# Optimization experiments

Hardware: AMD Instinct MI355X
Metric: run time of the kernel (lower is better)

The kernel has to match this reference:

```python
import math
import jax, jax.numpy as jnp
import numpy as np

B, L, D_M, H, D_K, D_V = 2, 2048, 1024, 16, 64, 64


def setup_inputs() -> dict:
    key = jax.random.key(0)
    ks = jax.random.split(key, 12)
    s_in = 1.0 / math.sqrt(D_M)
    s_cat = 1.0 / math.sqrt(H * D_V)
    return {
        "Q": jax.random.normal(ks[0], (B, L, D_M), jnp.float32),
        "K": jax.random.normal(ks[1], (B, L, D_M), jnp.float32),
        "V": jax.random.normal(ks[2], (B, L, D_M), jnp.float32),
        # per-head projections batched along a leading head axis
        "Wq": jax.random.uniform(ks[3], (H, D_M, D_K), jnp.float32, -s_in, s_in),
        "bq": jax.random.uniform(ks[4], (H, D_K), jnp.float32, -s_in, s_in),
        "Wk": jax.random.uniform(ks[5], (H, D_M, D_K), jnp.float32, -s_in, s_in),
        "bk": jax.random.uniform(ks[6], (H, D_K), jnp.float32, -s_in, s_in),
        "Wv": jax.random.uniform(ks[7], (H, D_M, D_V), jnp.float32, -s_in, s_in),
        "bv": jax.random.uniform(ks[8], (H, D_V), jnp.float32, -s_in, s_in),
        "Wo": jax.random.uniform(ks[9], (H * D_V, D_M), jnp.float32, -s_cat, s_cat),
        "bo": jax.random.uniform(ks[10], (D_M,), jnp.float32, -s_cat, s_cat),
    }


def reference(Q, K, V, Wq, bq, Wk, bk, Wv, bv, Wo, bo):
    # Batched per-head projections: [B,L,Dm] x [H,Dm,Dk] -> [B,H,L,Dk]
    Qp = jnp.einsum("bqm,hmk->bhqk", Q, Wq) + bq[None, :, None, :]
    Kp = jnp.einsum("bsm,hmk->bhsk", K, Wk) + bk[None, :, None, :]
    Vp = jnp.einsum("bsm,hmv->bhsv", V, Wv) + bv[None, :, None, :]
    scores = jnp.einsum("bhqk,bhsk->bhqs", Qp, Kp) / jnp.sqrt(
        jnp.asarray(D_K, Qp.dtype)
    )
    # NOTE: original torch code uses Softmax(dim=1) on a [B,Lq,Lk] matrix,
    # i.e. normalization over the QUERY axis (axis=2 here), not the key axis.
    attn = jax.nn.softmax(scores, axis=2)
    wV = jnp.einsum("bhqs,bhsv->bhqv", attn, Vp)  # [B,H,Lq,Dv]
    cat_V = jnp.transpose(wV, (0, 2, 1, 3)).reshape(B, L, H * D_V)
    return cat_V @ Wo + bo
```

## Files before the change

### kernel.cpp

```cpp
#include <hip/hip_runtime.h>
#include <hip/hip_bf16.h>

#define DEVI __device__ __forceinline__

typedef __hip_bfloat16 bf16;
typedef __attribute__((ext_vector_type(8))) __bf16 bf16x8;
typedef __attribute__((ext_vector_type(4))) float f32x4;
typedef __attribute__((ext_vector_type(4))) short short4v;
typedef __attribute__((ext_vector_type(8))) short short8v;


DEVI short bfbits(float f) { bf16 h = __float2bfloat16(f); return *(short*)&h; }

DEVI void gl16(const void* g, void* l) {
  __builtin_amdgcn_global_load_lds((const __attribute__((address_space(1))) void*)g,
                                   (__attribute__((address_space(3))) void*)l, 16, 0, 0);
}

DEVI f32x4 MF(bf16x8 a, bf16x8 b, f32x4 c) {
  return __builtin_amdgcn_mfma_f32_16x16x32_bf16(a, b, c, 0, 0, 0);
}

__global__ __launch_bounds__(256) void k_cvt_qkv(
    const float* __restrict__ Q, const float* __restrict__ K, const float* __restrict__ V,
    bf16* __restrict__ Qb, bf16* __restrict__ Kb, bf16* __restrict__ Vb) {
  const float* s = blockIdx.y == 0 ? Q : (blockIdx.y == 1 ? K : V);
  bf16* d = blockIdx.y == 0 ? Qb : (blockIdx.y == 1 ? Kb : Vb);
  int i = (blockIdx.x * 256 + threadIdx.x) * 4;
  float4 v = *(const float4*)(s + i);
  short4v o;
  o[0] = bfbits(v.x); o[1] = bfbits(v.y); o[2] = bfbits(v.z); o[3] = bfbits(v.w);
  *(short4v*)(d + i) = o;
}

__global__ __launch_bounds__(256) void k_prep_w(
    const float* __restrict__ Wq, const float* __restrict__ Wk, const float* __restrict__ Wv,
    const float* __restrict__ Wo,
    bf16* __restrict__ WqT, bf16* __restrict__ WkT, bf16* __restrict__ WvT,
    bf16* __restrict__ WoT) {
  __shared__ float t[64][65];
  const int z = blockIdx.z;
  const float* in; bf16* out; int ldin, ldout;
  if (z < 3) {
    const float* W = z == 0 ? Wq : (z == 1 ? Wk : Wv);
    bf16* O = z == 0 ? WqT : (z == 1 ? WkT : WvT);
    const int hh = blockIdx.y, m0 = blockIdx.x * 64;
    in = W + hh * 65536 + m0 * 64; ldin = 64;
    out = O + hh * 65536 + m0;     ldout = 1024;
  } else {
    const int r0 = blockIdx.x * 64, c0 = blockIdx.y * 64;
    in = Wo + r0 * 1024 + c0; ldin = 1024;
    out = WoT + c0 * 1024 + r0; ldout = 1024;
  }
  const int tx = threadIdx.x & 63, ty = threadIdx.x >> 6;
  for (int r = ty; r < 64; r += 4) t[r][tx] = in[r * ldin + tx];
  __syncthreads();
  for (int c = ty; c < 64; c += 4) out[c * ldout + tx] = __float2bfloat16(t[tx][c]);
}

__global__ __launch_bounds__(256) void k_proj_gemm(
    const bf16* __restrict__ Qb, const bf16* __restrict__ Kb, const bf16* __restrict__ Vb,
    const bf16* __restrict__ WqT, const bf16* __restrict__ WkT, const bf16* __restrict__ WvT,
    const float* __restrict__ bq, const float* __restrict__ bk, const float* __restrict__ bv,
    bf16* __restrict__ Qp, bf16* __restrict__ Kp, bf16* __restrict__ VpT) {
  __shared__ bf16 As[128 * 64], Bs[128 * 64];
  const int z = blockIdx.z;
  const bf16* A  = z == 0 ? Qb : (z == 1 ? Kb : Vb);
  const bf16* BT = z == 0 ? WqT : (z == 1 ? WkT : WvT);
  const float* bias = z == 0 ? bq : (z == 1 ? bk : bv);
  const int row0 = blockIdx.x * 128, col0 = blockIdx.y * 128;
  const int tid = threadIdx.x, lane = tid & 63, wave = tid >> 6;
  const int wq = wave >> 1, wn = wave & 1;
  f32x4 acc[4][4];
#pragma unroll
  for (int i = 0; i < 4; ++i)
#pragma unroll
    for (int j = 0; j < 4; ++j) acc[i][j] = (f32x4)0.0f;

  for (int k0 = 0; k0 < 1024; k0 += 64) {
#pragma unroll
    for (int it = 0; it < 4; ++it) {
      int boff = (it * 4 + wave) * 1024 + lane * 16;
      int r = boff >> 7, cb = boff & 127;
      gl16((const char*)A  + (size_t)(row0 + r) * 2048 + k0 * 2 + cb, (char*)As + boff);
      gl16((const char*)BT + (size_t)(col0 + r) * 2048 + k0 * 2 + cb, (char*)Bs + boff);
    }
    __syncthreads();
#pragma unroll
    for (int ks = 0; ks < 2; ++ks) {
      bf16x8 a[4], b[4];
#pragma unroll
      for (int i = 0; i < 4; ++i)
        a[i] = *(const bf16x8*)&As[(wq * 64 + i * 16 + (lane & 15)) * 64 + ks * 32 + (lane >> 4) * 8];
#pragma unroll
      for (int j = 0; j < 4; ++j)
        b[j] = *(const bf16x8*)&Bs[(wn * 64 + j * 16 + (lane & 15)) * 64 + ks * 32 + (lane >> 4) * 8];
#pragma unroll
      for (int i = 0; i < 4; ++i)
#pragma unroll
        for (int j = 0; j < 4; ++j) acc[i][j] = MF(a[i], b[j], acc[i][j]);
    }
    __syncthreads();
  }

  if (z < 2) {
    bf16* C = z == 0 ? Qp : Kp;
#pragma unroll
    for (int i = 0; i < 4; ++i)
#pragma unroll
      for (int j = 0; j < 4; ++j) {
        int col = col0 + wn * 64 + j * 16 + (lane & 15);
        float bb = bias[col];
#pragma unroll
        for (int r = 0; r < 4; ++r) {
          int row = row0 + wq * 64 + i * 16 + (lane >> 4) * 4 + r;
          C[row * 1024 + col] = __float2bfloat16(acc[i][j][r] + bb);
        }
      }
  } else {
    const int b = row0 >> 11, lr = row0 & 2047;
#pragma unroll
    for (int i = 0; i < 4; ++i)
#pragma unroll
      for (int j = 0; j < 4; ++j) {
        int n = col0 + wn * 64 + j * 16 + (lane & 15);
        float bb = bias[n];
        int s0 = lr + wq * 64 + i * 16 + (lane >> 4) * 4;
        short4v o;
#pragma unroll
        for (int r = 0; r < 4; ++r) o[r] = bfbits(acc[i][j][r] + bb);
        *(short4v*)&VpT[((b * 16 + (n >> 6)) * 64 + (n & 63)) * 2048 + s0] = o;
      }
  }
}

__global__ __launch_bounds__(256) void k_stats(
    const bf16* __restrict__ Qp, const bf16* __restrict__ Kp, float* __restrict__ lc) {
  __shared__ bf16 Ks[128 * 64], Qs[64 * 64];
  const int s0 = blockIdx.x * 128, bh = blockIdx.y;
  const int b = bh >> 4, h = bh & 15;
  const char* Qrow = (const char*)(Qp + (b * 2048) * 1024 + h * 64);
  const char* Krow = (const char*)(Kp + (b * 2048) * 1024 + h * 64);
  const int tid = threadIdx.x, lane = tid & 63, wave = tid >> 6;
#pragma unroll
  for (int it = 0; it < 4; ++it) {
    int boff = (it * 4 + wave) * 1024 + lane * 16;
    int r = boff >> 7, cb = boff & 127;
    gl16(Krow + (size_t)(s0 + r) * 2048 + cb, (char*)Ks + boff);
  }
  __syncthreads();
  bf16x8 afr[2][2];
#pragma unroll
  for (int sf = 0; sf < 2; ++sf)
#pragma unroll
    for (int ks = 0; ks < 2; ++ks)
      afr[sf][ks] = *(const bf16x8*)&Ks[(wave * 32 + sf * 16 + (lane & 15)) * 64 + ks * 32 + (lane >> 4) * 8];
  float zr[2][4] = {{0.f, 0.f, 0.f, 0.f}, {0.f, 0.f, 0.f, 0.f}};

  for (int q0 = 0; q0 < 2048; q0 += 64) {
    __syncthreads();
#pragma unroll
    for (int it = 0; it < 2; ++it) {
      int boff = (it * 4 + wave) * 1024 + lane * 16;
      int r = boff >> 7, cb = boff & 127;
      gl16(Qrow + (size_t)(q0 + r) * 2048 + cb, (char*)Qs + boff);
    }
    __syncthreads();
    f32x4 acc[2][4];
#pragma unroll
    for (int sf = 0; sf < 2; ++sf)
#pragma unroll
      for (int qf = 0; qf < 4; ++qf) acc[sf][qf] = (f32x4)0.0f;
#pragma unroll
    for (int ks = 0; ks < 2; ++ks) {
      bf16x8 bfr[4];
#pragma unroll
      for (int qf = 0; qf < 4; ++qf)
        bfr[qf] = *(const bf16x8*)&Qs[(qf * 16 + (lane & 15)) * 64 + ks * 32 + (lane >> 4) * 8];
#pragma unroll
      for (int sf = 0; sf < 2; ++sf)
#pragma unroll
        for (int qf = 0; qf < 4; ++qf) acc[sf][qf] = MF(afr[sf][ks], bfr[qf], acc[sf][qf]);
    }
#pragma unroll
    for (int sf = 0; sf < 2; ++sf)
#pragma unroll
      for (int qf = 0; qf < 4; ++qf)
#pragma unroll
        for (int r = 0; r < 4; ++r) zr[sf][r] += __expf(acc[sf][qf][r] * 0.125f);
  }
#pragma unroll
  for (int m = 1; m <= 8; m <<= 1)
#pragma unroll
    for (int sf = 0; sf < 2; ++sf)
#pragma unroll
      for (int r = 0; r < 4; ++r) zr[sf][r] += __shfl_xor(zr[sf][r], m);
  if ((lane & 15) == 0) {
#pragma unroll
    for (int sf = 0; sf < 2; ++sf)
#pragma unroll
      for (int r = 0; r < 4; ++r)
        lc[bh * 2048 + s0 + wave * 32 + sf * 16 + (lane >> 4) * 4 + r] = -__logf(zr[sf][r]);
  }
}

__global__ __launch_bounds__(256) void k_attn_pv(
    const bf16* __restrict__ Qp, const bf16* __restrict__ Kp, const bf16* __restrict__ VpT,
    const float* __restrict__ lc, bf16* __restrict__ wV) {
  __shared__ bf16 Qs[128 * 64];
  __shared__ bf16 Ks[64 * 64];
  __shared__ bf16 Vs[64 * 64];
  __shared__ bf16 Ps[128 * 72];
  __shared__ float lcs[64];
  const int q0 = blockIdx.x * 128, bh = blockIdx.y;
  const int b = bh >> 4, h = bh & 15;
  const char* Qrow = (const char*)(Qp + (b * 2048) * 1024 + h * 64);
  const char* Krow = (const char*)(Kp + (b * 2048) * 1024 + h * 64);
  const char* Vrow = (const char*)(VpT + bh * 64 * 2048);
  const float* lcb = lc + bh * 2048;
  const int tid = threadIdx.x, lane = tid & 63, wave = tid >> 6;

#pragma unroll
  for (int it = 0; it < 4; ++it) {
    int boff = (it * 4 + wave) * 1024 + lane * 16;
    int r = boff >> 7, cb = boff & 127;
    gl16(Qrow + (size_t)(q0 + r) * 2048 + cb, (char*)Qs + boff);
  }
  __syncthreads();
  bf16x8 aq[2][2];
#pragma unroll
  for (int qf = 0; qf < 2; ++qf)
#pragma unroll
    for (int ks = 0; ks < 2; ++ks)
      aq[qf][ks] = *(const bf16x8*)&Qs[(wave * 32 + qf * 16 + (lane & 15)) * 64 + ks * 32 + (lane >> 4) * 8];

  f32x4 acco[2][4];
#pragma unroll
  for (int qf = 0; qf < 2; ++qf)
#pragma unroll
    for (int vf = 0; vf < 4; ++vf) acco[qf][vf] = (f32x4)0.0f;

  for (int sc = 0; sc < 2048; sc += 64) {
    __syncthreads();
#pragma unroll
    for (int it = 0; it < 2; ++it) {
      int boff = (it * 4 + wave) * 1024 + lane * 16;
      int r = boff >> 7, cb = boff & 127;
      gl16(Krow + (size_t)(sc + r) * 2048 + cb, (char*)Ks + boff);
      gl16(Vrow + (size_t)r * 4096 + sc * 2 + cb, (char*)Vs + boff);
    }
    if (tid < 64) lcs[tid] = lcb[sc + tid];
    __syncthreads();

    f32x4 sacc[2][4];
#pragma unroll
    for (int qf = 0; qf < 2; ++qf)
#pragma unroll
      for (int sf = 0; sf < 4; ++sf) sacc[qf][sf] = (f32x4)0.0f;
#pragma unroll
    for (int ks = 0; ks < 2; ++ks) {
      bf16x8 bk_[4];
#pragma unroll
      for (int sf = 0; sf < 4; ++sf)
        bk_[sf] = *(const bf16x8*)&Ks[(sf * 16 + (lane & 15)) * 64 + ks * 32 + (lane >> 4) * 8];
#pragma unroll
      for (int qf = 0; qf < 2; ++qf)
#pragma unroll
        for (int sf = 0; sf < 4; ++sf) sacc[qf][sf] = MF(aq[qf][ks], bk_[sf], sacc[qf][sf]);
    }
#pragma unroll
    for (int qf = 0; qf < 2; ++qf)
#pragma unroll
      for (int sf = 0; sf < 4; ++sf) {
        int sl = sf * 16 + (lane & 15);
        float lcv = lcs[sl];
#pragma unroll
        for (int r = 0; r < 4; ++r) {
          float p = __expf(sacc[qf][sf][r] * 0.125f + lcv);
          Ps[(wave * 32 + qf * 16 + (lane >> 4) * 4 + r) * 72 + sl] = __float2bfloat16(p);
        }
      }
#pragma unroll
    for (int ks = 0; ks < 2; ++ks) {
      bf16x8 pa[2], pb[4];
#pragma unroll
      for (int qf = 0; qf < 2; ++qf)
        pa[qf] = *(const bf16x8*)&Ps[(wave * 32 + qf * 16 + (lane & 15)) * 72 + ks * 32 + (lane >> 4) * 8];
#pragma unroll
      for (int vf = 0; vf < 4; ++vf)
        pb[vf] = *(const bf16x8*)&Vs[(vf * 16 + (lane & 15)) * 64 + ks * 32 + (lane >> 4) * 8];
#pragma unroll
      for (int qf = 0; qf < 2; ++qf)
#pragma unroll
        for (int vf = 0; vf < 4; ++vf) acco[qf][vf] = MF(pa[qf], pb[vf], acco[qf][vf]);
    }
  }
#pragma unroll
  for (int qf = 0; qf < 2; ++qf)
#pragma unroll
    for (int vf = 0; vf < 4; ++vf) {
      int v = vf * 16 + (lane & 15);
#pragma unroll
      for (int r = 0; r < 4; ++r)
        Ps[(wave * 32 + qf * 16 + (lane >> 4) * 4 + r) * 72 + v] = __float2bfloat16(acco[qf][vf][r]);
    }
  __syncthreads();
  {
    int r = tid >> 1, p = tid & 1;
    char* dst = (char*)(wV + (bh * 2048 + q0 + r) * 64 + p * 32);
#pragma unroll
    for (int i = 0; i < 4; ++i) {
      short8v x = *(const short8v*)&Ps[r * 72 + p * 32 + i * 8];
      *(short8v*)(dst + i * 16) = x;
    }
  }
}

__global__ __launch_bounds__(256) void k_out_gemm(
    const bf16* __restrict__ wV, const bf16* __restrict__ WoT, const float* __restrict__ bo,
    float* __restrict__ out) {
  __shared__ bf16 As[128 * 64], Bs[128 * 64];
  const int row0 = blockIdx.x * 128, col0 = blockIdx.y * 128;
  const int tid = threadIdx.x, lane = tid & 63, wave = tid >> 6;
  const int wq = wave >> 1, wn = wave & 1;
  const int b = row0 >> 11, lr = row0 & 2047;
  f32x4 acc[4][4];
#pragma unroll
  for (int i = 0; i < 4; ++i)
#pragma unroll
    for (int j = 0; j < 4; ++j) acc[i][j] = (f32x4)0.0f;

  for (int k0 = 0; k0 < 1024; k0 += 64) {
    const char* Abase = (const char*)(wV + ((b * 16 + (k0 >> 6)) * 2048 + lr) * 64);
#pragma unroll
    for (int it = 0; it < 4; ++it) {
      int boff = (it * 4 + wave) * 1024 + lane * 16;
      int r = boff >> 7, cb = boff & 127;
      gl16(Abase + boff, (char*)As + boff);
      gl16((const char*)WoT + (size_t)(col0 + r) * 2048 + k0 * 2 + cb, (char*)Bs + boff);
    }
    __syncthreads();
#pragma unroll
    for (int ks = 0; ks < 2; ++ks) {
      bf16x8 a[4], bb[4];
#pragma unroll
      for (int i = 0; i < 4; ++i)
        a[i] = *(const bf16x8*)&As[(wq * 64 + i * 16 + (lane & 15)) * 64 + ks * 32 + (lane >> 4) * 8];
#pragma unroll
      for (int j = 0; j < 4; ++j)
        bb[j] = *(const bf16x8*)&Bs[(wn * 64 + j * 16 + (lane & 15)) * 64 + ks * 32 + (lane >> 4) * 8];
#pragma unroll
      for (int i = 0; i < 4; ++i)
#pragma unroll
        for (int j = 0; j < 4; ++j) acc[i][j] = MF(a[i], bb[j], acc[i][j]);
    }
    __syncthreads();
  }
#pragma unroll
  for (int i = 0; i < 4; ++i)
#pragma unroll
    for (int j = 0; j < 4; ++j) {
      int col = col0 + wn * 64 + j * 16 + (lane & 15);
      float bb = bo[col];
#pragma unroll
      for (int r = 0; r < 4; ++r) {
        int row = row0 + wq * 64 + i * 16 + (lane >> 4) * 4 + r;
        out[row * 1024 + col] = acc[i][j][r] + bb;
      }
    }
}

extern "C" void kernel_launch(void* const* d_in, const int* in_sizes, int n_in,
                              void* d_out, int out_size, void* d_ws, size_t ws_size,
                              hipStream_t stream) {
  (void)in_sizes; (void)n_in; (void)out_size; (void)ws_size;
  const float* Q  = (const float*)d_in[0];
  const float* K  = (const float*)d_in[1];
  const float* V  = (const float*)d_in[2];
  const float* Wq = (const float*)d_in[3];
  const float* bq = (const float*)d_in[4];
  const float* Wk = (const float*)d_in[5];
  const float* bk = (const float*)d_in[6];
  const float* Wv = (const float*)d_in[7];
  const float* bv = (const float*)d_in[8];
  const float* Wo = (const float*)d_in[9];
  const float* bo = (const float*)d_in[10];

  char* ws = (char*)d_ws;
  bf16* Qb  = (bf16*)(ws);
  bf16* Kb  = (bf16*)(ws + (8u  << 20));
  bf16* Vb  = (bf16*)(ws + (16u << 20));
  bf16* WqT = (bf16*)(ws + (24u << 20));
  bf16* WkT = (bf16*)(ws + (26u << 20));
  bf16* WvT = (bf16*)(ws + (28u << 20));
  bf16* WoT = (bf16*)(ws + (30u << 20));
  bf16* Qp  = (bf16*)(ws + (32u << 20));
  bf16* Kp  = (bf16*)(ws + (40u << 20));
  bf16* VpT = (bf16*)(ws + (48u << 20));
  bf16* wVn = (bf16*)(ws + (56u << 20));
  float* lc = (float*)(ws + (64u << 20));

  k_cvt_qkv <<<dim3(4096, 3), 256, 0, stream>>>(Q, K, V, Qb, Kb, Vb);
  k_prep_w  <<<dim3(16, 16, 4), 256, 0, stream>>>(Wq, Wk, Wv, Wo, WqT, WkT, WvT, WoT);
  k_proj_gemm<<<dim3(32, 8, 3), 256, 0, stream>>>(Qb, Kb, Vb, WqT, WkT, WvT, bq, bk, bv, Qp, Kp, VpT);
  k_stats   <<<dim3(16, 32), 256, 0, stream>>>(Qp, Kp, lc);
  k_attn_pv <<<dim3(16, 32), 256, 0, stream>>>(Qp, Kp, VpT, lc, wVn);
  k_out_gemm<<<dim3(32, 8), 256, 0, stream>>>(wVn, WoT, bo, (float*)d_out);
}
```

Baseline: 306.3 us.

## Swizzle LDS tiles, fold softmax normalizer into V, double-buffer attention kernels

Applies an XOR swizzle to all LDS tiles to avoid bank conflicts. Folds the 1/8 scale into Qp and moves the per-key normalizer into a rescale of VpT, so the attention kernel only computes exp(s). It also stages the VpT transpose through LDS for coalesced stores, double-buffers the K/V/Q tiles, and moves the attention kernels to 512-thread blocks with a swizzled block order. The risks are skipping max-subtraction in exp, which could overflow on other inputs, and an extra bf16 rounding of V.

Result: faster. 262.5 us (-14.3%).

```diff
diff --git a/kernel.cpp b/kernel.cpp
--- a/kernel.cpp
+++ b/kernel.cpp
@@ -11,6 +11,7 @@
 
 
 DEVI short bfbits(float f) { bf16 h = __float2bfloat16(f); return *(short*)&h; }
+DEVI float b2f(short s) { union { float f; unsigned u; } c; c.u = ((unsigned)(unsigned short)s) << 16; return c.f; }
 
 DEVI void gl16(const void* g, void* l) {
   __builtin_amdgcn_global_load_lds((const __attribute__((address_space(1))) void*)g,
@@ -20,6 +21,9 @@
 DEVI f32x4 MF(bf16x8 a, bf16x8 b, f32x4 c) {
   return __builtin_amdgcn_mfma_f32_16x16x32_bf16(a, b, c, 0, 0, 0);
 }
+
+DEVI int swzE(int row, int ec) { return row * 64 + (ec ^ ((row & 7) << 3)); }
+DEVI int srcC(int boff) { return (boff & 127) ^ (((boff >> 7) & 7) << 4); }
 
 __global__ __launch_bounds__(256) void k_cvt_qkv(
     const float* __restrict__ Q, const float* __restrict__ K, const float* __restrict__ V,
@@ -63,7 +67,9 @@
     const bf16* __restrict__ WqT, const bf16* __restrict__ WkT, const bf16* __restrict__ WvT,
     const float* __restrict__ bq, const float* __restrict__ bk, const float* __restrict__ bv,
     bf16* __restrict__ Qp, bf16* __restrict__ Kp, bf16* __restrict__ VpT) {
-  __shared__ bf16 As[128 * 64], Bs[128 * 64];
+  __shared__ bf16 smem[17408];
+  bf16* As = smem;
+  bf16* Bs = smem + 8192;
   const int z = blockIdx.z;
   const bf16* A  = z == 0 ? Qb : (z == 1 ? Kb : Vb);
   const bf16* BT = z == 0 ? WqT : (z == 1 ? WkT : WvT);
@@ -81,9 +87,9 @@
 #pragma unroll
     for (int it = 0; it < 4; ++it) {
       int boff = (it * 4 + wave) * 1024 + lane * 16;
-      int r = boff >> 7, cb = boff & 127;
-      gl16((const char*)A  + (size_t)(row0 + r) * 2048 + k0 * 2 + cb, (char*)As + boff);
-      gl16((const char*)BT + (size_t)(col0 + r) * 2048 + k0 * 2 + cb, (char*)Bs + boff);
+      int r = boff >> 7, c = srcC(boff);
+      gl16((const char*)A  + (size_t)(row0 + r) * 2048 + k0 * 2 + c, (char*)As + boff);
+      gl16((const char*)BT + (size_t)(col0 + r) * 2048 + k0 * 2 + c, (char*)Bs + boff);
     }
     __syncthreads();
 #pragma unroll
@@ -91,10 +97,10 @@
       bf16x8 a[4], b[4];
 #pragma unroll
       for (int i = 0; i < 4; ++i)
-        a[i] = *(const bf16x8*)&As[(wq * 64 + i * 16 + (lane & 15)) * 64 + ks * 32 + (lane >> 4) * 8];
+        a[i] = *(const bf16x8*)&As[swzE(wq * 64 + i * 16 + (lane & 15), ks * 32 + (lane >> 4) * 8)];
 #pragma unroll
       for (int j = 0; j < 4; ++j)
-        b[j] = *(const bf16x8*)&Bs[(wn * 64 + j * 16 + (lane & 15)) * 64 + ks * 32 + (lane >> 4) * 8];
+        b[j] = *(const bf16x8*)&Bs[swzE(wn * 64 + j * 16 + (lane & 15), ks * 32 + (lane >> 4) * 8)];
 #pragma unroll
       for (int i = 0; i < 4; ++i)
 #pragma unroll
@@ -104,6 +110,7 @@
   }
 
   if (z < 2) {
+    const float scl = (z == 0) ? 0.125f : 1.0f;
     bf16* C = z == 0 ? Qp : Kp;
 #pragma unroll
     for (int i = 0; i < 4; ++i)
@@ -114,205 +121,203 @@
 #pragma unroll
         for (int r = 0; r < 4; ++r) {
           int row = row0 + wq * 64 + i * 16 + (lane >> 4) * 4 + r;
-          C[row * 1024 + col] = __float2bfloat16(acc[i][j][r] + bb);
+          C[row * 1024 + col] = __float2bfloat16((acc[i][j][r] + bb) * scl);
         }
       }
   } else {
+    bf16* T = smem;
+#pragma unroll
+    for (int i = 0; i < 4; ++i)
+#pragma unroll
+      for (int j = 0; j < 4; ++j) {
+        int nl = wn * 64 + j * 16 + (lane & 15);
+        float bb = bias[col0 + nl];
+#pragma unroll
+        for (int r = 0; r < 4; ++r) {
+          int sl = wq * 64 + i * 16 + (lane >> 4) * 4 + r;
+          T[nl * 136 + sl] = __float2bfloat16(acc[i][j][r] + bb);
+        }
+      }
+    __syncthreads();
     const int b = row0 >> 11, lr = row0 & 2047;
-#pragma unroll
-    for (int i = 0; i < 4; ++i)
-#pragma unroll
-      for (int j = 0; j < 4; ++j) {
-        int n = col0 + wn * 64 + j * 16 + (lane & 15);
-        float bb = bias[n];
-        int s0 = lr + wq * 64 + i * 16 + (lane >> 4) * 4;
-        short4v o;
-#pragma unroll
-        for (int r = 0; r < 4; ++r) o[r] = bfbits(acc[i][j][r] + bb);
-        *(short4v*)&VpT[((b * 16 + (n >> 6)) * 64 + (n & 63)) * 2048 + s0] = o;
-      }
-  }
-}
-
-__global__ __launch_bounds__(256) void k_stats(
-    const bf16* __restrict__ Qp, const bf16* __restrict__ Kp, float* __restrict__ lc) {
-  __shared__ bf16 Ks[128 * 64], Qs[64 * 64];
-  const int s0 = blockIdx.x * 128, bh = blockIdx.y;
+    const int nl = tid >> 1, half = tid & 1;
+    const int n = col0 + nl;
+    bf16* drow = VpT + ((size_t)(b * 16 + (n >> 6)) * 64 + (n & 63)) * 2048 + lr + half * 64;
+#pragma unroll
+    for (int k = 0; k < 8; ++k)
+      *(short8v*)(drow + k * 8) = *(const short8v*)&T[nl * 136 + half * 64 + k * 8];
+  }
+}
+
+__global__ __launch_bounds__(512, 4) void k_stats(
+    const bf16* __restrict__ Qp, const bf16* __restrict__ Kp, bf16* __restrict__ VpT) {
+  __shared__ bf16 Ks[128 * 64];
+  __shared__ bf16 Qs[2][64 * 64];
+  __shared__ float zs[128];
+  const int id = blockIdx.x;
+  const int sw = (id & 7) * 64 + (id >> 3);
+  const int bh = sw >> 4, s0 = (sw & 15) * 128;
   const int b = bh >> 4, h = bh & 15;
-  const char* Qrow = (const char*)(Qp + (b * 2048) * 1024 + h * 64);
-  const char* Krow = (const char*)(Kp + (b * 2048) * 1024 + h * 64);
+  const char* Qrow = (const char*)(Qp + (size_t)(b * 2048) * 1024 + h * 64);
+  const char* Krow = (const char*)(Kp + (size_t)(b * 2048) * 1024 + h * 64);
   const int tid = threadIdx.x, lane = tid & 63, wave = tid >> 6;
-#pragma unroll
-  for (int it = 0; it < 4; ++it) {
-    int boff = (it * 4 + wave) * 1024 + lane * 16;
-    int r = boff >> 7, cb = boff & 127;
-    gl16(Krow + (size_t)(s0 + r) * 2048 + cb, (char*)Ks + boff);
+
+  {
+    int boff = tid * 16;
+#pragma unroll
+    for (int it = 0; it < 2; ++it) {
+      int bo = boff + it * 8192;
+      gl16(Krow + (size_t)(s0 + (bo >> 7)) * 2048 + srcC(bo), (char*)Ks + bo);
+    }
+    gl16(Qrow + (size_t)(boff >> 7) * 2048 + srcC(boff), (char*)Qs[0] + boff);
   }
   __syncthreads();
-  bf16x8 afr[2][2];
-#pragma unroll
-  for (int sf = 0; sf < 2; ++sf)
-#pragma unroll
-    for (int ks = 0; ks < 2; ++ks)
-      afr[sf][ks] = *(const bf16x8*)&Ks[(wave * 32 + sf * 16 + (lane & 15)) * 64 + ks * 32 + (lane >> 4) * 8];
-  float zr[2][4] = {{0.f, 0.f, 0.f, 0.f}, {0.f, 0.f, 0.f, 0.f}};
-
-  for (int q0 = 0; q0 < 2048; q0 += 64) {
-    __syncthreads();
-#pragma unroll
-    for (int it = 0; it < 2; ++it) {
-      int boff = (it * 4 + wave) * 1024 + lane * 16;
-      int r = boff >> 7, cb = boff & 127;
-      gl16(Qrow + (size_t)(q0 + r) * 2048 + cb, (char*)Qs + boff);
-    }
-    __syncthreads();
-    f32x4 acc[2][4];
-#pragma unroll
-    for (int sf = 0; sf < 2; ++sf)
-#pragma unroll
-      for (int qf = 0; qf < 4; ++qf) acc[sf][qf] = (f32x4)0.0f;
+  bf16x8 afr[2];
+#pragma unroll
+  for (int ks = 0; ks < 2; ++ks)
+    afr[ks] = *(const bf16x8*)&Ks[swzE(wave * 16 + (lane & 15), ks * 32 + (lane >> 4) * 8)];
+
+  float zr[4] = {0.f, 0.f, 0.f, 0.f};
+  for (int c = 0; c < 32; ++c) {
+    const int p = c & 1;
+    if (c < 31) {
+      int boff = tid * 16;
+      gl16(Qrow + (size_t)((c + 1) * 64 + (boff >> 7)) * 2048 + srcC(boff), (char*)Qs[p ^ 1] + boff);
+    }
+    f32x4 acc[4];
+#pragma unroll
+    for (int qf = 0; qf < 4; ++qf) acc[qf] = (f32x4)0.0f;
 #pragma unroll
     for (int ks = 0; ks < 2; ++ks) {
       bf16x8 bfr[4];
 #pragma unroll
       for (int qf = 0; qf < 4; ++qf)
-        bfr[qf] = *(const bf16x8*)&Qs[(qf * 16 + (lane & 15)) * 64 + ks * 32 + (lane >> 4) * 8];
-#pragma unroll
-      for (int sf = 0; sf < 2; ++sf)
-#pragma unroll
-        for (int qf = 0; qf < 4; ++qf) acc[sf][qf] = MF(afr[sf][ks], bfr[qf], acc[sf][qf]);
-    }
-#pragma unroll
-    for (int sf = 0; sf < 2; ++sf)
-#pragma unroll
-      for (int qf = 0; qf < 4; ++qf)
-#pragma unroll
-        for (int r = 0; r < 4; ++r) zr[sf][r] += __expf(acc[sf][qf][r] * 0.125f);
+        bfr[qf] = *(const bf16x8*)&Qs[p][swzE(qf * 16 + (lane & 15), ks * 32 + (lane >> 4) * 8)];
+#pragma unroll
+      for (int qf = 0; qf < 4; ++qf) acc[qf] = MF(afr[ks], bfr[qf], acc[qf]);
+    }
+#pragma unroll
+    for (int qf = 0; qf < 4; ++qf)
+#pragma unroll
+      for (int r = 0; r < 4; ++r) zr[r] += __expf(acc[qf][r]);
+    __syncthreads();
   }
 #pragma unroll
   for (int m = 1; m <= 8; m <<= 1)
 #pragma unroll
-    for (int sf = 0; sf < 2; ++sf)
-#pragma unroll
-      for (int r = 0; r < 4; ++r) zr[sf][r] += __shfl_xor(zr[sf][r], m);
+    for (int r = 0; r < 4; ++r) zr[r] += __shfl_xor(zr[r], m);
   if ((lane & 15) == 0) {
 #pragma unroll
-    for (int sf = 0; sf < 2; ++sf)
-#pragma unroll
-      for (int r = 0; r < 4; ++r)
-        lc[bh * 2048 + s0 + wave * 32 + sf * 16 + (lane >> 4) * 4 + r] = -__logf(zr[sf][r]);
-  }
-}
-
-__global__ __launch_bounds__(256) void k_attn_pv(
+    for (int r = 0; r < 4; ++r) zs[wave * 16 + (lane >> 4) * 4 + r] = 1.0f / zr[r];
+  }
+  __syncthreads();
+  {
+    const int v = tid >> 3, seg = tid & 7;
+    bf16* base = VpT + (size_t)(bh * 64 + v) * 2048 + s0 + seg * 16;
+    short8v x0 = *(const short8v*)base;
+    short8v x1 = *(const short8v*)(base + 8);
+    short8v o0, o1;
+#pragma unroll
+    for (int j = 0; j < 8; ++j) {
+      o0[j] = bfbits(b2f(x0[j]) * zs[seg * 16 + j]);
+      o1[j] = bfbits(b2f(x1[j]) * zs[seg * 16 + 8 + j]);
+    }
+    *(short8v*)base = o0;
+    *(short8v*)(base + 8) = o1;
+  }
+}
+
+__global__ __launch_bounds__(512, 4) void k_attn_pv(
     const bf16* __restrict__ Qp, const bf16* __restrict__ Kp, const bf16* __restrict__ VpT,
-    const float* __restrict__ lc, bf16* __restrict__ wV) {
-  __shared__ bf16 Qs[128 * 64];
-  __shared__ bf16 Ks[64 * 64];
-  __shared__ bf16 Vs[64 * 64];
-  __shared__ bf16 Ps[128 * 72];
-  __shared__ float lcs[64];
-  const int q0 = blockIdx.x * 128, bh = blockIdx.y;
+    bf16* __restrict__ wV) {
+  __shared__ bf16 QPs[128 * 64];
+  __shared__ bf16 Ks[2][64 * 64];
+  __shared__ bf16 Vs[2][64 * 64];
+  const int id = blockIdx.x;
+  const int sw = (id & 7) * 64 + (id >> 3);
+  const int bh = sw >> 4, q0 = (sw & 15) * 128;
   const int b = bh >> 4, h = bh & 15;
-  const char* Qrow = (const char*)(Qp + (b * 2048) * 1024 + h * 64);
-  const char* Krow = (const char*)(Kp + (b * 2048) * 1024 + h * 64);
-  const char* Vrow = (const char*)(VpT + bh * 64 * 2048);
-  const float* lcb = lc + bh * 2048;
+  const char* Qrow = (const char*)(Qp + (size_t)(b * 2048) * 1024 + h * 64);
+  const char* Krow = (const char*)(Kp + (size_t)(b * 2048) * 1024 + h * 64);
+  const char* Vrow = (const char*)(VpT + (size_t)bh * 64 * 2048);
   const int tid = threadIdx.x, lane = tid & 63, wave = tid >> 6;
 
-#pragma unroll
-  for (int it = 0; it < 4; ++it) {
-    int boff = (it * 4 + wave) * 1024 + lane * 16;
-    int r = boff >> 7, cb = boff & 127;
-    gl16(Qrow + (size_t)(q0 + r) * 2048 + cb, (char*)Qs + boff);
+  {
+    int boff = tid * 16;
+#pragma unroll
+    for (int it = 0; it < 2; ++it) {
+      int bo = boff + it * 8192;
+      gl16(Qrow + (size_t)(q0 + (bo >> 7)) * 2048 + srcC(bo), (char*)QPs + bo);
+    }
+    gl16(Krow + (size_t)(boff >> 7) * 2048 + srcC(boff), (char*)Ks[0] + boff);
+    gl16(Vrow + (size_t)(boff >> 7) * 4096 + srcC(boff), (char*)Vs[0] + boff);
   }
   __syncthreads();
-  bf16x8 aq[2][2];
-#pragma unroll
-  for (int qf = 0; qf < 2; ++qf)
-#pragma unroll
-    for (int ks = 0; ks < 2; ++ks)
-      aq[qf][ks] = *(const bf16x8*)&Qs[(wave * 32 + qf * 16 + (lane & 15)) * 64 + ks * 32 + (lane >> 4) * 8];
-
-  f32x4 acco[2][4];
-#pragma unroll
-  for (int qf = 0; qf < 2; ++qf)
-#pragma unroll
-    for (int vf = 0; vf < 4; ++vf) acco[qf][vf] = (f32x4)0.0f;
-
-  for (int sc = 0; sc < 2048; sc += 64) {
-    __syncthreads();
-#pragma unroll
-    for (int it = 0; it < 2; ++it) {
-      int boff = (it * 4 + wave) * 1024 + lane * 16;
-      int r = boff >> 7, cb = boff & 127;
-      gl16(Krow + (size_t)(sc + r) * 2048 + cb, (char*)Ks + boff);
-      gl16(Vrow + (size_t)r * 4096 + sc * 2 + cb, (char*)Vs + boff);
-    }
-    if (tid < 64) lcs[tid] = lcb[sc + tid];
-    __syncthreads();
-
-    f32x4 sacc[2][4];
-#pragma unroll
-    for (int qf = 0; qf < 2; ++qf)
-#pragma unroll
-      for (int sf = 0; sf < 4; ++sf) sacc[qf][sf] = (f32x4)0.0f;
+  bf16x8 aq[2];
+#pragma unroll
+  for (int ks = 0; ks < 2; ++ks)
+    aq[ks] = *(const bf16x8*)&QPs[swzE(wave * 16 + (lane & 15), ks * 32 + (lane >> 4) * 8)];
+
+  f32x4 acco[4];
+#pragma unroll
+  for (int vf = 0; vf < 4; ++vf) acco[vf] = (f32x4)0.0f;
+
+  for (int c = 0; c < 32; ++c) {
+    const int p = c & 1;
+    if (c < 31) {
+      int boff = tid * 16;
+      gl16(Krow + (size_t)((c + 1) * 64 + (boff >> 7)) * 2048 + srcC(boff), (char*)Ks[p ^ 1] + boff);
+      gl16(Vrow + (size_t)(boff >> 7) * 4096 + (c + 1) * 128 + srcC(boff), (char*)Vs[p ^ 1] + boff);
+    }
+    f32x4 sacc[4];
+#pragma unroll
+    for (int sf = 0; sf < 4; ++sf) sacc[sf] = (f32x4)0.0f;
 #pragma unroll
     for (int ks = 0; ks < 2; ++ks) {
       bf16x8 bk_[4];
 #pragma unroll
       for (int sf = 0; sf < 4; ++sf)
-        bk_[sf] = *(const bf16x8*)&Ks[(sf * 16 + (lane & 15)) * 64 + ks * 32 + (lane >> 4) * 8];
-#pragma unroll
-      for (int qf = 0; qf < 2; ++qf)
-#pragma unroll
-        for (int sf = 0; sf < 4; ++sf) sacc[qf][sf] = MF(aq[qf][ks], bk_[sf], sacc[qf][sf]);
-    }
-#pragma unroll
-    for (int qf = 0; qf < 2; ++qf)
-#pragma unroll
-      for (int sf = 0; sf < 4; ++sf) {
-        int sl = sf * 16 + (lane & 15);
-        float lcv = lcs[sl];
-#pragma unroll
-        for (int r = 0; r < 4; ++r) {
-          float p = __expf(sacc[qf][sf][r] * 0.125f + lcv);
-          Ps[(wave * 32 + qf * 16 + (lane >> 4) * 4 + r) * 72 + sl] = __float2bfloat16(p);
-        }
+        bk_[sf] = *(const bf16x8*)&Ks[p][swzE(sf * 16 + (lane & 15), ks * 32 + (lane >> 4) * 8)];
+#pragma unroll
+      for (int sf = 0; sf < 4; ++sf) sacc[sf] = MF(aq[ks], bk_[sf], sacc[sf]);
+    }
+#pragma unroll
+    for (int sf = 0; sf < 4; ++sf) {
+      int sl = sf * 16 + (lane & 15);
+#pragma unroll
+      for (int r = 0; r < 4; ++r) {
+        int row = wave * 16 + (lane >> 4) * 4 + r;
+        QPs[swzE(row, sl)] = __float2bfloat16(__expf(sacc[sf][r]));
       }
+    }
 #pragma unroll
     for (int ks = 0; ks < 2; ++ks) {
-      bf16x8 pa[2], pb[4];
-#pragma unroll
-      for (int qf = 0; qf < 2; ++qf)
-        pa[qf] = *(const bf16x8*)&Ps[(wave * 32 + qf * 16 + (lane & 15)) * 72 + ks * 32 + (lane >> 4) * 8];
+      bf16x8 pa = *(const bf16x8*)&QPs[swzE(wave * 16 + (lane & 15), ks * 32 + (lane >> 4) * 8)];
+      bf16x8 pb[4];
 #pragma unroll
       for (int vf = 0; vf < 4; ++vf)
-        pb[vf] = *(const bf16x8*)&Vs[(vf * 16 + (lane & 15)) * 64 + ks * 32 + (lane >> 4) * 8];
-#pragma unroll
-      for (int qf = 0; qf < 2; ++qf)
-#pragma unroll
-        for (int vf = 0; vf < 4; ++vf) acco[qf][vf] = MF(pa[qf], pb[vf], acco[qf][vf]);
-    }
-  }
-#pragma unroll
-  for (int qf = 0; qf < 2; ++qf)
-#pragma unroll
-    for (int vf = 0; vf < 4; ++vf) {
-      int v = vf * 16 + (lane & 15);
-#pragma unroll
-      for (int r = 0; r < 4; ++r)
-        Ps[(wave * 32 + qf * 16 + (lane >> 4) * 4 + r) * 72 + v] = __float2bfloat16(acco[qf][vf][r]);
-    }
-  __syncthreads();
+        pb[vf] = *(const bf16x8*)&Vs[p][swzE(vf * 16 + (lane & 15), ks * 32 + (lane >> 4) * 8)];
+#pragma unroll
+      for (int vf = 0; vf < 4; ++vf) acco[vf] = MF(pa, pb[vf], acco[vf]);
+    }
+    __syncthreads();
+  }
+
+#pragma unroll
+  for (int vf = 0; vf < 4; ++vf) {
+    int v = vf * 16 + (lane & 15);
+#pragma unroll
+    for (int r = 0; r < 4; ++r)
+      QPs[swzE(wave * 16 + (lane >> 4) * 4 + r, v)] = __float2bfloat16(acco[vf][r]);
+  }
   {
-    int r = tid >> 1, p = tid & 1;
-    char* dst = (char*)(wV + (bh * 2048 + q0 + r) * 64 + p * 32);
-#pragma unroll
-    for (int i = 0; i < 4; ++i) {
-      short8v x = *(const short8v*)&Ps[r * 72 + p * 32 + i * 8];
-      *(short8v*)(dst + i * 16) = x;
-    }
+    const int rr = wave * 16 + (lane >> 2);
+    const int x = (rr & 7) << 3;
+    short8v x0 = *(const short8v*)&QPs[rr * 64 + (((lane & 3) * 16) ^ x)];
+    short8v x1 = *(const short8v*)&QPs[rr * 64 + (((lane & 3) * 16 + 8) ^ x)];
+    bf16* dst = wV + ((size_t)bh * 2048 + q0 + rr) * 64 + (lane & 3) * 16;
+    *(short8v*)dst = x0;
+    *(short8v*)(dst + 8) = x1;
   }
 }
 
@@ -331,13 +336,13 @@
     for (int j = 0; j < 4; ++j) acc[i][j] = (f32x4)0.0f;
 
   for (int k0 = 0; k0 < 1024; k0 += 64) {
-    const char* Abase = (const char*)(wV + ((b * 16 + (k0 >> 6)) * 2048 + lr) * 64);
+    const char* Abase = (const char*)(wV + ((size_t)(b * 16 + (k0 >> 6)) * 2048 + lr) * 64);
 #pragma unroll
     for (int it = 0; it < 4; ++it) {
       int boff = (it * 4 + wave) * 1024 + lane * 16;
-      int r = boff >> 7, cb = boff & 127;
-      gl16(Abase + boff, (char*)As + boff);
-      gl16((const char*)WoT + (size_t)(col0 + r) * 2048 + k0 * 2 + cb, (char*)Bs + boff);
+      int r = boff >> 7, c = srcC(boff);
+      gl16(Abase + (size_t)r * 128 + c, (char*)As + boff);
+      gl16((const char*)WoT + (size_t)(col0 + r) * 2048 + k0 * 2 + c, (char*)Bs + boff);
     }
     __syncthreads();
 #pragma unroll
@@ -345,10 +350,10 @@
       bf16x8 a[4], bb[4];
 #pragma unroll
       for (int i = 0; i < 4; ++i)
-        a[i] = *(const bf16x8*)&As[(wq * 64 + i * 16 + (lane & 15)) * 64 + ks * 32 + (lane >> 4) * 8];
+        a[i] = *(const bf16x8*)&As[swzE(wq * 64 + i * 16 + (lane & 15), ks * 32 + (lane >> 4) * 8)];
 #pragma unroll
       for (int j = 0; j < 4; ++j)
-        bb[j] = *(const bf16x8*)&Bs[(wn * 64 + j * 16 + (lane & 15)) * 64 + ks * 32 + (lane >> 4) * 8];
+        bb[j] = *(const bf16x8*)&Bs[swzE(wn * 64 + j * 16 + (lane & 15), ks * 32 + (lane >> 4) * 8)];
 #pragma unroll
       for (int i = 0; i < 4; ++i)
 #pragma unroll
@@ -398,12 +403,11 @@
   bf16* Kp  = (bf16*)(ws + (40u << 20));
   bf16* VpT = (bf16*)(ws + (48u << 20));
   bf16* wVn = (bf16*)(ws + (56u << 20));
-  float* lc = (float*)(ws + (64u << 20));
 
   k_cvt_qkv <<<dim3(4096, 3), 256, 0, stream>>>(Q, K, V, Qb, Kb, Vb);
   k_prep_w  <<<dim3(16, 16, 4), 256, 0, stream>>>(Wq, Wk, Wv, Wo, WqT, WkT, WvT, WoT);
   k_proj_gemm<<<dim3(32, 8, 3), 256, 0, stream>>>(Qb, Kb, Vb, WqT, WkT, WvT, bq, bk, bv, Qp, Kp, VpT);
-  k_stats   <<<dim3(16, 32), 256, 0, stream>>>(Qp, Kp, lc);
-  k_attn_pv <<<dim3(16, 32), 256, 0, stream>>>(Qp, Kp, VpT, lc, wVn);
+  k_stats   <<<512, 512, 0, stream>>>(Qp, Kp, VpT);
+  k_attn_pv <<<512, 512, 0, stream>>>(Qp, Kp, VpT, wVn);
   k_out_gemm<<<dim3(32, 8), 256, 0, stream>>>(wVn, WoT, bo, (float*)d_out);
 }
```
